# Performance work log

Measured on AMD Instinct MI355X. Metric: run time of the kernel, lower is better.

Reference implementation:

```python
import jax, jax.numpy as jnp
import numpy as np

N, C, K = 300000, 64, 27  # active voxels, channels, 3^3 kernel offsets


def sparse_conv(x, nbr, mask, W, b):
    """MinkowskiConvolution as gather -> GEMM -> accumulate.
    x: [N, C] features; nbr: [N, K] int32 neighbor index per kernel offset;
    mask: [N, K] bool validity; W: [K, C, C]; b: [C].
    out[i] = b + sum_k mask[i,k] * x[nbr[i,k]] @ W[k]
    Scans over the K=27 fixed kernel offsets so only an [N, C] gathered
    buffer is live at a time (never materializes [N, K, C]).
    """
    def step(acc, kin):
        Wk, nk, mk = kin
        g = jnp.where(mk[:, None], x[nk], jnp.zeros((), x.dtype))  # [N, C] gather
        return acc + g @ Wk, None

    acc0 = jnp.zeros_like(x) + b
    out, _ = jax.lax.scan(step, acc0, (W, nbr.T, mask.T))
    return out


def setup_inputs() -> dict:
    key = jax.random.key(0)
    ks = jax.random.split(key, 7)
    features = jax.random.normal(ks[0], (N, C), dtype=jnp.float32)
    neighbor_idx = jax.random.randint(ks[1], (N, K), 0, N, dtype=jnp.int32)
    neighbor_mask = jax.random.uniform(ks[2], (N, K)) < 0.6  # variable neighbor counts
    scale = 1.0 / np.sqrt(K * C)
    W0 = jax.random.normal(ks[3], (K, C, C), dtype=jnp.float32) * scale
    b0 = jax.random.normal(ks[4], (C,), dtype=jnp.float32) * 0.01
    W1 = jax.random.normal(ks[5], (K, C, C), dtype=jnp.float32) * scale
    b1 = jax.random.normal(ks[6], (C,), dtype=jnp.float32) * 0.01
    return {
        "features": features,
        "neighbor_idx": neighbor_idx,
        "neighbor_mask": neighbor_mask,
        "W0": W0, "b0": b0, "W1": W1, "b1": b1,
    }


def reference(features, neighbor_idx, neighbor_mask, W0, b0, W1, b1):
    # conv0 -> ReLU -> conv1 -> residual add (stride=1, shared kernel map)
    out = sparse_conv(features, neighbor_idx, neighbor_mask, W0, b0)
    out = jax.nn.relu(out)
    out = sparse_conv(out, neighbor_idx, neighbor_mask, W1, b1)
    return out + features
```

## Files before the change

### kernel.cpp

```cpp
#include <hip/hip_runtime.h>
#include <hip/hip_bf16.h>
#include <stdint.h>

typedef __bf16 bf16x8 __attribute__((ext_vector_type(8)));
typedef float f32x4 __attribute__((ext_vector_type(4)));
typedef unsigned short u16x4 __attribute__((ext_vector_type(4)));

__device__ __forceinline__ unsigned short f2bf(float f) {
    union { float f; uint32_t u; } v; v.f = f;
    uint32_t u = v.u;
    return (unsigned short)((u + 0x7fffu + ((u >> 16) & 1u)) >> 16);
}

__device__ __forceinline__ float bf2f(unsigned short b) {
    union { uint32_t u; float f; } v; v.u = ((uint32_t)b) << 16;
    return v.f;
}

__global__ __launch_bounds__(256) void prep_x(const f32x4* __restrict__ x,
                                              u16x4* __restrict__ xb, int n4, int n4tot) {
    int t = blockIdx.x * 256 + threadIdx.x;
    if (t < n4) {
        f32x4 v = x[t];
        u16x4 o;
        o.x = f2bf(v.x); o.y = f2bf(v.y); o.z = f2bf(v.z); o.w = f2bf(v.w);
        xb[t] = o;
    } else if (t < n4tot) {
        u16x4 z = {0, 0, 0, 0};
        xb[t] = z;
    }
}

__global__ void zero_row(unsigned short* __restrict__ p, long off) {
    p[off + threadIdx.x] = 0;
}

__global__ __launch_bounds__(256) void prep_w(const float* __restrict__ W,
                                              unsigned short* __restrict__ Wf) {
    int k = blockIdx.x;
    unsigned short* Wfk = Wf + (size_t)k * 4096;
    const float* Wk = W + (size_t)k * 4096;
    for (int idx = threadIdx.x; idx < 4096; idx += 256) {
        int j   = idx & 7;
        int l   = (idx >> 3) & 63;
        int c2h = idx >> 9;
        int ct  = c2h >> 1, h = c2h & 1;
        int ci  = h * 32 + (l >> 4) * 8 + j;
        int co  = ct * 16 + (l & 15);
        Wfk[idx] = f2bf(Wk[ci * 64 + co]);
    }
}

__global__ void detect_mask(const unsigned int* __restrict__ m, int* __restrict__ flag) {
    __shared__ int s_not_int, s_not_f32;
    if (threadIdx.x == 0) { s_not_int = 0; s_not_f32 = 0; }
    __syncthreads();
    unsigned int w = m[threadIdx.x];
    if (w > 1u) s_not_int = 1;
    if (w != 0u && w != 0x3f800000u) s_not_f32 = 1;
    __syncthreads();
    if (threadIdx.x == 0) *flag = s_not_int ? (s_not_f32 ? 1 : 2) : 0;
}

template <int IOFF>
__device__ __forceinline__ bf16x8 gl16(const unsigned short* base, unsigned voff) {
    bf16x8 r;
    asm volatile("global_load_dwordx4 %0, %1, %2 offset:%c3"
                 : "=v"(r) : "v"(voff), "s"(base), "i"(IOFF));
    return r;
}

struct Slot { bf16x8 f[8]; };

template <int NW>
__device__ __forceinline__ void waitv(Slot& s) {
    asm volatile("s_waitcnt vmcnt(%c8)"
                 : "+v"(s.f[0]), "+v"(s.f[1]), "+v"(s.f[2]), "+v"(s.f[3]),
                   "+v"(s.f[4]), "+v"(s.f[5]), "+v"(s.f[6]), "+v"(s.f[7])
                 : "i"(NW));
    __builtin_amdgcn_sched_barrier(0);
}

__device__ __forceinline__ void gload_lds16(const unsigned short* g, unsigned short* l) {
    __builtin_amdgcn_global_load_lds(
        (const __attribute__((address_space(1))) void*)(const void*)g,
        (__attribute__((address_space(3))) void*)(void*)l, 16, 0, 0);
}

template <int MODE>
__global__ __launch_bounds__(256, 2) void conv_mfma(
    const unsigned short* __restrict__ xb,
    const int* __restrict__ nbr,
    const void* __restrict__ maskp,
    const int* __restrict__ flagp,
    const unsigned short* __restrict__ Wf,
    const float* __restrict__ bias,
    const unsigned short* __restrict__ residb,
    void* __restrict__ outp,
    int N, int K)
{
    __shared__ unsigned short Wlds[16384];

    const int tid = threadIdx.x;
    const int wv  = tid >> 6;
    const int l   = tid & 63;
    const int lr  = l & 15;
    const int lg  = l >> 4;
    const int wavebase = blockIdx.x * 256 + wv * 64;

    const int myrow = wavebase + l;
    const int mr = myrow < N ? myrow : N - 1;

    unsigned mbits = 0;
    {
        const int flag = *flagp;
        long moff = (long)mr * K;
        if (flag == 1) {
            const unsigned char* mp = (const unsigned char*)maskp + moff;
#pragma unroll
            for (int k = 0; k < 27; ++k) mbits |= (mp[k] ? 1u : 0u) << k;
        } else if (flag == 0) {
            const int* mp = (const int*)maskp + moff;
#pragma unroll
            for (int k = 0; k < 27; ++k) mbits |= (mp[k] ? 1u : 0u) << k;
        } else {
            const float* mp = (const float*)maskp + moff;
#pragma unroll
            for (int k = 0; k < 27; ++k) mbits |= ((mp[k] != 0.f) ? 1u : 0u) << k;
        }
    }

    unsigned o[27];
    {
        const int* nrow = nbr + (long)mr * K;
#pragma unroll
        for (int k = 0; k < 27; ++k) {
            unsigned g = ((mbits >> k) & 1u) ? (unsigned)nrow[k] : (unsigned)N;
            o[k] = g * 128u;
        }
    }

    const int bpa0 = (0 * 16 + lr) * 4;
    const int bpa1 = (1 * 16 + lr) * 4;
    const int bpa2 = (2 * 16 + lr) * 4;
    const int bpa3 = (3 * 16 + lr) * 4;
    const unsigned chk = (unsigned)(lg << 4);

    f32x4 acc[4][4] = {};
    Slot pipe[2];
    bf16x8 Bf[8];

#define STAGE(P) do { \
    const unsigned short* _src = Wf + (size_t)(P) * 8192 + wv * 2048 + (l << 3); \
    unsigned short* _dst = &Wlds[((P) & 1) * 8192 + wv * 2048]; \
    _Pragma("unroll") \
    for (int _s = 0; _s < 4; ++_s) \
        gload_lds16(_src + _s * 512, _dst + _s * 512); \
    asm volatile("" ::: "memory"); \
} while (0)

#define STAGE1(P) do { \
    const unsigned short* _src = Wf + (size_t)(P) * 8192 + wv * 1024 + (l << 3); \
    unsigned short* _dst = &Wlds[((P) & 1) * 8192 + wv * 1024]; \
    _Pragma("unroll") \
    for (int _s = 0; _s < 2; ++_s) \
        gload_lds16(_src + _s * 512, _dst + _s * 512); \
    asm volatile("" ::: "memory"); \
} while (0)

#define GISSUE(J) do { \
    unsigned _b0 = (unsigned)__builtin_amdgcn_ds_bpermute(bpa0, (int)o[J]) + chk; \
    unsigned _b1 = (unsigned)__builtin_amdgcn_ds_bpermute(bpa1, (int)o[J]) + chk; \
    unsigned _b2 = (unsigned)__builtin_amdgcn_ds_bpermute(bpa2, (int)o[J]) + chk; \
    unsigned _b3 = (unsigned)__builtin_amdgcn_ds_bpermute(bpa3, (int)o[J]) + chk; \
    Slot& _s = pipe[(J) & 1]; \
    _s.f[0] = gl16<0 >(xb, _b0); _s.f[1] = gl16<64>(xb, _b0); \
    _s.f[2] = gl16<0 >(xb, _b1); _s.f[3] = gl16<64>(xb, _b1); \
    _s.f[4] = gl16<0 >(xb, _b2); _s.f[5] = gl16<64>(xb, _b2); \
    _s.f[6] = gl16<0 >(xb, _b3); _s.f[7] = gl16<64>(xb, _b3); \
} while (0)

#define BLOAD(J) do { \
    const unsigned short* _wl = &Wlds[(((J) >> 1) & 1) * 8192 + ((J) & 1) * 4096]; \
    _Pragma("unroll") \
    for (int _c = 0; _c < 8; ++_c) \
        Bf[_c] = *(const bf16x8*)(_wl + _c * 512 + l * 8); \
} while (0)

#define MFMA16(J) do { \
    Slot& _s = pipe[(J) & 1]; \
    _Pragma("unroll") \
    for (int ct = 0; ct < 4; ++ct) { \
        _Pragma("unroll") \
        for (int at = 0; at < 4; ++at) { \
            acc[at][ct] = __builtin_amdgcn_mfma_f32_16x16x32_bf16(_s.f[at * 2],     Bf[ct * 2],     acc[at][ct], 0, 0, 0); \
            acc[at][ct] = __builtin_amdgcn_mfma_f32_16x16x32_bf16(_s.f[at * 2 + 1], Bf[ct * 2 + 1], acc[at][ct], 0, 0, 0); \
        } \
    } \
} while (0)

#define FENCE(NW) do { \
    asm volatile("s_waitcnt vmcnt(%c0)" :: "i"(NW) : "memory"); \
    __builtin_amdgcn_sched_barrier(0); \
    __builtin_amdgcn_s_barrier(); \
    __builtin_amdgcn_sched_barrier(0); \
} while (0)

#define STEP(J, NW) do { BLOAD(J); waitv<NW>(pipe[(J) & 1]); MFMA16(J); } while (0)

#define PHASE(PH1, K0) do { \
    STAGE(PH1); \
    STEP(K0, 12);       GISSUE((K0) + 2); \
    STEP((K0) + 1, 12); GISSUE((K0) + 3); \
    FENCE(16); \
} while (0)

    STAGE(0);
    GISSUE(0); GISSUE(1);
    asm volatile("s_waitcnt vmcnt(16)" ::: "memory");
    __builtin_amdgcn_sched_barrier(0);
    __builtin_amdgcn_s_barrier();
    __builtin_amdgcn_sched_barrier(0);

    PHASE(1, 0);   PHASE(2, 2);   PHASE(3, 4);   PHASE(4, 6);
    PHASE(5, 8);   PHASE(6, 10);  PHASE(7, 12);  PHASE(8, 14);
    PHASE(9, 16);  PHASE(10, 18); PHASE(11, 20); PHASE(12, 22);
    STAGE1(13);
    STEP(24, 10); GISSUE(26);
    STEP(25, 10);
    FENCE(8);
    STEP(26, 0);

#pragma unroll
    for (int at = 0; at < 4; ++at) {
#pragma unroll
        for (int ct = 0; ct < 4; ++ct) {
            int col = ct * 16 + lr;
            float bv = bias[col];
#pragma unroll
            for (int rg = 0; rg < 4; ++rg) {
                int row = wavebase + at * 16 + lg * 4 + rg;
                if (row < N) {
                    long oo = (long)row * 64 + col;
                    float v = acc[at][ct][rg] + bv;
                    if (MODE == 0) {
                        ((unsigned short*)outp)[oo] = f2bf(v > 0.f ? v : 0.f);
                    } else {
                        ((float*)outp)[oo] = v + bf2f(residb[oo]);
                    }
                }
            }
        }
    }

#undef STAGE
#undef STAGE1
#undef GISSUE
#undef BLOAD
#undef MFMA16
#undef FENCE
#undef STEP
#undef PHASE
}

static inline size_t align256(size_t x) { return (x + 255) & ~(size_t)255; }

extern "C" void kernel_launch(void* const* d_in, const int* in_sizes, int n_in,
                              void* d_out, int out_size, void* d_ws, size_t ws_size,
                              hipStream_t stream) {
    const float* x    = (const float*)d_in[0];
    const int*   nbr  = (const int*)d_in[1];
    const void*  mask = d_in[2];
    const float* W0   = (const float*)d_in[3];
    const float* b0   = (const float*)d_in[4];
    const float* W1   = (const float*)d_in[5];
    const float* b1   = (const float*)d_in[6];

    const int NC = in_sizes[0];
    const int N  = NC / 64;
    const int K  = in_sizes[1] / N;

    char* ws = (char*)d_ws;
    size_t xb_bytes = (size_t)(NC + 64) * 2;
    size_t wt_bytes = (size_t)28 * 4096 * 2;
    size_t xb_off   = 0;
    size_t hb_off   = xb_off + align256(xb_bytes);
    size_t wt0_off  = hb_off + align256(xb_bytes);
    size_t wt1_off  = wt0_off + align256(wt_bytes);
    size_t flag_off = wt1_off + align256(wt_bytes);

    unsigned short* xb  = (unsigned short*)(ws + xb_off);
    unsigned short* hb  = (unsigned short*)(ws + hb_off);
    unsigned short* wf0 = (unsigned short*)(ws + wt0_off);
    unsigned short* wf1 = (unsigned short*)(ws + wt1_off);
    int* flag           = (int*)(ws + flag_off);

    int n4 = NC / 4;
    int n4tot = n4 + 16;
    prep_x<<<(n4tot + 255) / 256, 256, 0, stream>>>((const f32x4*)x, (u16x4*)xb, n4, n4tot);
    zero_row<<<1, 64, 0, stream>>>(hb, (long)NC);
    prep_w<<<27, 256, 0, stream>>>(W0, wf0);
    prep_w<<<27, 256, 0, stream>>>(W1, wf1);
    detect_mask<<<1, 1024, 0, stream>>>((const unsigned int*)mask, flag);

    int nblocks = (N + 255) / 256;
    conv_mfma<0><<<nblocks, 256, 0, stream>>>(xb, nbr, mask, flag, wf0, b0, nullptr, hb, N, K);
    conv_mfma<1><<<nblocks, 256, 0, stream>>>(hb, nbr, mask, flag, wf1, b1, xb, d_out, N, K);
}
```

Measured before the change: 331.9 us.

## Halve rows per wave to 32 and raise occupancy to four blocks per CU

```diff
diff --git a/kernel.cpp b/kernel.cpp
--- a/kernel.cpp
+++ b/kernel.cpp
@@ -70,13 +70,12 @@
     return r;
 }
 
-struct Slot { bf16x8 f[8]; };
+struct Slot { bf16x8 f[4]; };
 
 template <int NW>
 __device__ __forceinline__ void waitv(Slot& s) {
-    asm volatile("s_waitcnt vmcnt(%c8)"
-                 : "+v"(s.f[0]), "+v"(s.f[1]), "+v"(s.f[2]), "+v"(s.f[3]),
-                   "+v"(s.f[4]), "+v"(s.f[5]), "+v"(s.f[6]), "+v"(s.f[7])
+    asm volatile("s_waitcnt vmcnt(%c4)"
+                 : "+v"(s.f[0]), "+v"(s.f[1]), "+v"(s.f[2]), "+v"(s.f[3])
                  : "i"(NW));
     __builtin_amdgcn_sched_barrier(0);
 }
@@ -88,7 +87,7 @@
 }
 
 template <int MODE>
-__global__ __launch_bounds__(256, 2) void conv_mfma(
+__global__ __launch_bounds__(256, 4) void conv_mfma(
     const unsigned short* __restrict__ xb,
     const int* __restrict__ nbr,
     const void* __restrict__ maskp,
@@ -106,9 +105,9 @@
     const int l   = tid & 63;
     const int lr  = l & 15;
     const int lg  = l >> 4;
-    const int wavebase = blockIdx.x * 256 + wv * 64;
-
-    const int myrow = wavebase + l;
+    const int wavebase = blockIdx.x * 128 + wv * 32;
+
+    const int myrow = wavebase + (l & 31);
     const int mr = myrow < N ? myrow : N - 1;
 
     unsigned mbits = 0;
@@ -142,13 +141,11 @@
 
     const int bpa0 = (0 * 16 + lr) * 4;
     const int bpa1 = (1 * 16 + lr) * 4;
-    const int bpa2 = (2 * 16 + lr) * 4;
-    const int bpa3 = (3 * 16 + lr) * 4;
     const unsigned chk = (unsigned)(lg << 4);
 
-    f32x4 acc[4][4] = {};
+    f32x4 acc[2][4] = {};
     Slot pipe[2];
-    bf16x8 Bf[8];
+    bf16x8 Bf[4];
 
 #define STAGE(P) do { \
     const unsigned short* _src = Wf + (size_t)(P) * 8192 + wv * 2048 + (l << 3); \
@@ -171,30 +168,27 @@
 #define GISSUE(J) do { \
     unsigned _b0 = (unsigned)__builtin_amdgcn_ds_bpermute(bpa0, (int)o[J]) + chk; \
     unsigned _b1 = (unsigned)__builtin_amdgcn_ds_bpermute(bpa1, (int)o[J]) + chk; \
-    unsigned _b2 = (unsigned)__builtin_amdgcn_ds_bpermute(bpa2, (int)o[J]) + chk; \
-    unsigned _b3 = (unsigned)__builtin_amdgcn_ds_bpermute(bpa3, (int)o[J]) + chk; \
     Slot& _s = pipe[(J) & 1]; \
     _s.f[0] = gl16<0 >(xb, _b0); _s.f[1] = gl16<64>(xb, _b0); \
     _s.f[2] = gl16<0 >(xb, _b1); _s.f[3] = gl16<64>(xb, _b1); \
-    _s.f[4] = gl16<0 >(xb, _b2); _s.f[5] = gl16<64>(xb, _b2); \
-    _s.f[6] = gl16<0 >(xb, _b3); _s.f[7] = gl16<64>(xb, _b3); \
-} while (0)
-
-#define BLOAD(J) do { \
+} while (0)
+
+#define BLOADH(J, CP) do { \
     const unsigned short* _wl = &Wlds[(((J) >> 1) & 1) * 8192 + ((J) & 1) * 4096]; \
     _Pragma("unroll") \
-    for (int _c = 0; _c < 8; ++_c) \
-        Bf[_c] = *(const bf16x8*)(_wl + _c * 512 + l * 8); \
-} while (0)
-
-#define MFMA16(J) do { \
+    for (int _c = 0; _c < 4; ++_c) \
+        Bf[_c] = *(const bf16x8*)(_wl + ((CP) * 4 + _c) * 512 + l * 8); \
+} while (0)
+
+#define MFMA8(J, CP) do { \
     Slot& _s = pipe[(J) & 1]; \
     _Pragma("unroll") \
-    for (int ct = 0; ct < 4; ++ct) { \
+    for (int _q = 0; _q < 2; ++_q) { \
+        int ct = (CP) * 2 + _q; \
         _Pragma("unroll") \
-        for (int at = 0; at < 4; ++at) { \
-            acc[at][ct] = __builtin_amdgcn_mfma_f32_16x16x32_bf16(_s.f[at * 2],     Bf[ct * 2],     acc[at][ct], 0, 0, 0); \
-            acc[at][ct] = __builtin_amdgcn_mfma_f32_16x16x32_bf16(_s.f[at * 2 + 1], Bf[ct * 2 + 1], acc[at][ct], 0, 0, 0); \
+        for (int at = 0; at < 2; ++at) { \
+            acc[at][ct] = __builtin_amdgcn_mfma_f32_16x16x32_bf16(_s.f[at * 2],     Bf[_q * 2],     acc[at][ct], 0, 0, 0); \
+            acc[at][ct] = __builtin_amdgcn_mfma_f32_16x16x32_bf16(_s.f[at * 2 + 1], Bf[_q * 2 + 1], acc[at][ct], 0, 0, 0); \
         } \
     } \
 } while (0)
@@ -206,18 +200,21 @@
     __builtin_amdgcn_sched_barrier(0); \
 } while (0)
 
-#define STEP(J, NW) do { BLOAD(J); waitv<NW>(pipe[(J) & 1]); MFMA16(J); } while (0)
+#define STEP(J, NW) do { \
+    BLOADH(J, 0); waitv<NW>(pipe[(J) & 1]); MFMA8(J, 0); \
+    BLOADH(J, 1); MFMA8(J, 1); \
+} while (0)
 
 #define PHASE(PH1, K0) do { \
     STAGE(PH1); \
-    STEP(K0, 12);       GISSUE((K0) + 2); \
-    STEP((K0) + 1, 12); GISSUE((K0) + 3); \
-    FENCE(16); \
+    STEP(K0, 8);       GISSUE((K0) + 2); \
+    STEP((K0) + 1, 8); GISSUE((K0) + 3); \
+    FENCE(8); \
 } while (0)
 
     STAGE(0);
     GISSUE(0); GISSUE(1);
-    asm volatile("s_waitcnt vmcnt(16)" ::: "memory");
+    asm volatile("s_waitcnt vmcnt(8)" ::: "memory");
     __builtin_amdgcn_sched_barrier(0);
     __builtin_amdgcn_s_barrier();
     __builtin_amdgcn_sched_barrier(0);
@@ -226,13 +223,13 @@
     PHASE(5, 8);   PHASE(6, 10);  PHASE(7, 12);  PHASE(8, 14);
     PHASE(9, 16);  PHASE(10, 18); PHASE(11, 20); PHASE(12, 22);
     STAGE1(13);
-    STEP(24, 10); GISSUE(26);
-    STEP(25, 10);
-    FENCE(8);
+    STEP(24, 6); GISSUE(26);
+    STEP(25, 6);
+    FENCE(4);
     STEP(26, 0);
 
 #pragma unroll
-    for (int at = 0; at < 4; ++at) {
+    for (int at = 0; at < 2; ++at) {
 #pragma unroll
         for (int ct = 0; ct < 4; ++ct) {
             int col = ct * 16 + lr;
@@ -256,8 +253,8 @@
 #undef STAGE
 #undef STAGE1
 #undef GISSUE
-#undef BLOAD
-#undef MFMA16
+#undef BLOADH
+#undef MFMA8
 #undef FENCE
 #undef STEP
 #undef PHASE
@@ -303,7 +300,7 @@
     prep_w<<<27, 256, 0, stream>>>(W1, wf1);
     detect_mask<<<1, 1024, 0, stream>>>((const unsigned int*)mask, flag);
 
-    int nblocks = (N + 255) / 256;
+    int nblocks = (N + 127) / 128;
     conv_mfma<0><<<nblocks, 256, 0, stream>>>(xb, nbr, mask, flag, wf0, b0, nullptr, hb, N, K);
     conv_mfma<1><<<nblocks, 256, 0, stream>>>(hb, nbr, mask, flag, wf1, b1, xb, d_out, N, K);
 }
```

Measured after the change: 323.1 us. -2.7%, faster.
